# Performance work log

Measured on AMD Instinct MI355X. Metric: run time of the kernel, lower is better.

The kernel has to match this reference:

```python
import jax, jax.numpy as jnp
import numpy as np

N_NODES = 100000
N_EDGES = 800000
IN_FEATS = 128
HIDDEN = 64
SCALE = 0.5 ** 0.5  # sqrt(0.5) residual scale
BN_EPS = 1e-5


def setup_inputs() -> dict:
    key = jax.random.key(0)
    ks = jax.random.split(key, 12)
    return {
        "src": jax.random.randint(ks[0], (N_EDGES,), 0, N_NODES, dtype=jnp.int64)
        if jax.config.jax_enable_x64 else jax.random.randint(ks[0], (N_EDGES,), 0, N_NODES),
        "dst": jax.random.randint(ks[1], (N_EDGES,), 0, N_NODES),
        "x": jax.random.normal(ks[2], (N_NODES, IN_FEATS), dtype=jnp.float32),
        "fc_w": jax.random.normal(ks[3], (IN_FEATS, HIDDEN), dtype=jnp.float32) * 0.05,
        "fc_b": jax.random.normal(ks[4], (HIDDEN,), dtype=jnp.float32) * 0.05,
        "w1": jax.random.normal(ks[5], (HIDDEN, HIDDEN), dtype=jnp.float32) * 0.05,
        "b1": jax.random.normal(ks[6], (HIDDEN,), dtype=jnp.float32) * 0.05,
        "w2": jax.random.normal(ks[7], (HIDDEN, HIDDEN), dtype=jnp.float32) * 0.05,
        "b2": jax.random.normal(ks[8], (HIDDEN,), dtype=jnp.float32) * 0.05,
        "gamma": jax.random.normal(ks[9], (HIDDEN,), dtype=jnp.float32) * 0.05 + 1.0,
        "beta": jax.random.normal(ks[10], (HIDDEN,), dtype=jnp.float32) * 0.05,
    }


def _graph_conv(h, w, b, src, dst, norm_src, norm_dst, n_nodes):
    # DGL GraphConv, norm='both': y = D_in^{-1/2} A D_out^{-1/2} (h W) + b
    h = h @ w                                   # [N, H]
    m = h[src] * norm_src[:, None]              # gather + src-degree norm, [E, H]
    agg = jax.ops.segment_sum(m, dst, num_segments=n_nodes)  # scatter-add, [N, H]
    return agg * norm_dst[:, None] + b


def reference(src, dst, x, fc_w, fc_b, w1, b1, w2, b2, gamma, beta):
    n_nodes = x.shape[0]
    ones_e = jnp.ones(src.shape[0], dtype=x.dtype)
    deg_out = jnp.clip(jax.ops.segment_sum(ones_e, src, num_segments=n_nodes), 1.0)
    deg_in = jnp.clip(jax.ops.segment_sum(ones_e, dst, num_segments=n_nodes), 1.0)
    norm_src = (deg_out ** -0.5)[src]           # per-edge source normalization
    norm_dst = deg_in ** -0.5                   # per-node destination normalization

    h = x @ fc_w + fc_b                          # fc: [N, H]
    h = (h + _graph_conv(h, w1, b1, src, dst, norm_src, norm_dst, n_nodes)) * SCALE
    h = (h + _graph_conv(h, w2, b2, src, dst, norm_src, norm_dst, n_nodes)) * SCALE

    # BatchNorm1d (training-mode batch statistics over nodes, biased variance)
    mu = h.mean(axis=0)
    var = ((h - mu) ** 2).mean(axis=0)
    h = (h - mu) * jax.lax.rsqrt(var + BN_EPS) * gamma + beta
    return h
```

## Files before the change

### kernel.cpp

```cpp
#include <hip/hip_runtime.h>

#define HIDDEN 64
#define INFEAT 128
#define SCALE_C 0.70710678118654752f
#define BN_EPS 1e-5f
#define AGG_GRID 2048
#define RED_BLK 32

__device__ __forceinline__ int rli(int v, int l){ return __builtin_amdgcn_readlane(v, l); }

template<int KDIM, bool ADDB, bool FUSET>
__device__ __forceinline__ void gemm_body(int bid, const float* __restrict__ X,
    const float* __restrict__ W, const float* __restrict__ B,
    float* __restrict__ Y, const float* __restrict__ W2, float* __restrict__ T, int N)
{
  __shared__ float smem[128 * 65];
  const int tid  = threadIdx.x;
  const int lane = tid & 63;
  const int wid  = __builtin_amdgcn_readfirstlane(tid >> 6);
  const int nodehalf = wid >> 1;
  const int c0 = (wid & 1) * 32;
  const int base = bid * 128;
  const int myNode = nodehalf * 64 + lane;
  const int gnode = base + myNode;

  float acc[32];
  #pragma unroll
  for (int c = 0; c < 32; ++c) acc[c] = ADDB ? B[c0 + c] : 0.f;

  constexpr int NCHUNK = KDIM / 32;
  #pragma unroll 1
  for (int ck = 0; ck < NCHUNK; ++ck){
    __syncthreads();
    #pragma unroll
    for (int i = 0; i < 4; ++i){
      int f  = i * 256 + tid;
      int nd = f >> 3;
      int kq = f & 7;
      float4 v = make_float4(0.f, 0.f, 0.f, 0.f);
      if (base + nd < N)
        v = *(const float4*)(X + (size_t)(base + nd) * KDIM + ck * 32 + kq * 4);
      float* p = &smem[nd * 33 + kq * 4];
      p[0] = v.x; p[1] = v.y; p[2] = v.z; p[3] = v.w;
    }
    __syncthreads();
    const float* wrow = W + (size_t)ck * 32 * HIDDEN + c0;
    #pragma unroll
    for (int k = 0; k < 32; ++k){
      float xv = smem[myNode * 33 + k];
      #pragma unroll
      for (int c = 0; c < 32; ++c)
        acc[c] = fmaf(xv, wrow[k * HIDDEN + c], acc[c]);
    }
  }

  if (gnode < N){
    float4* yp = (float4*)(Y + (size_t)gnode * HIDDEN + c0);
    #pragma unroll
    for (int j = 0; j < 8; ++j)
      yp[j] = make_float4(acc[4*j], acc[4*j+1], acc[4*j+2], acc[4*j+3]);
  }

  if constexpr (FUSET){
    __syncthreads();
    #pragma unroll
    for (int c = 0; c < 32; ++c)
      smem[myNode * 65 + c0 + c] = acc[c];
    __syncthreads();
    float tacc[32];
    #pragma unroll
    for (int c = 0; c < 32; ++c) tacc[c] = 0.f;
    const float* w2r = W2 + c0;
    #pragma unroll
    for (int k = 0; k < 64; ++k){
      float hv = smem[myNode * 65 + k];
      #pragma unroll
      for (int c = 0; c < 32; ++c)
        tacc[c] = fmaf(hv, w2r[k * HIDDEN + c], tacc[c]);
    }
    if (gnode < N){
      float4* tp = (float4*)(T + (size_t)gnode * HIDDEN + c0);
      #pragma unroll
      for (int j = 0; j < 8; ++j)
        tp[j] = make_float4(tacc[4*j], tacc[4*j+1], tacc[4*j+2], tacc[4*j+3]);
    }
  }
}

__device__ __forceinline__ int role_gemm_idx(int b, int GB, int TOT, int& histIdx){
  int fb  = (int)(((long)b * GB) / TOT);
  int fb1 = (int)(((long)(b + 1) * GB) / TOT);
  histIdx = b - fb;
  return (fb1 > fb) ? fb : -1;
}

__global__ __launch_bounds__(256) void k_mega1(const int* __restrict__ dst,
    int* __restrict__ degI, int* __restrict__ rank, int E,
    const float* __restrict__ x, const float* __restrict__ fc_w,
    const float* __restrict__ fc_b, float* __restrict__ h,
    const float* __restrict__ w1, float* __restrict__ t, int N, int GB, int TOT){
  int hIdx;
  int g = role_gemm_idx(blockIdx.x, GB, TOT, hIdx);
  if (g >= 0) gemm_body<INFEAT, true, true>(g, x, fc_w, fc_b, h, w1, t, N);
  else {
    int e = hIdx * 256 + threadIdx.x;
    if (e < E) rank[e] = atomicAdd(&degI[dst[e]], 1);
  }
}

__global__ __launch_bounds__(256) void k_place2(const int* __restrict__ src,
    const int* __restrict__ dst, const int* __restrict__ rank,
    const int* __restrict__ rp, int* __restrict__ cs, int* __restrict__ degO, int E){
  int e = (blockIdx.x >> 1) * 256 + threadIdx.x;
  if (e < E){
    if (blockIdx.x & 1) atomicAdd(&degO[src[e]], 1);
    else                cs[rp[dst[e]] + rank[e]] = src[e];
  }
}

__global__ __launch_bounds__(256) void k_gemm64(const float* __restrict__ X,
    const float* __restrict__ W, float* __restrict__ Y, int N){
  gemm_body<HIDDEN, false, false>(blockIdx.x, X, W, nullptr, Y, nullptr, nullptr, N);
}

__global__ void k_scan1(const int* __restrict__ deg, int* __restrict__ bsum, int N){
  __shared__ int sh[256];
  int t = threadIdx.x;
  int i = blockIdx.x * 256 + t;
  sh[t] = (i < N) ? deg[i] : 0;
  __syncthreads();
  for (int ofs = 128; ofs > 0; ofs >>= 1){
    if (t < ofs) sh[t] += sh[t + ofs];
    __syncthreads();
  }
  if (t == 0) bsum[blockIdx.x] = sh[0];
}

__global__ void k_scan2(int* __restrict__ bsum, int NB){
  __shared__ int sh[512];
  int t = threadIdx.x;
  int v = (t < NB) ? bsum[t] : 0;
  sh[t] = v;
  __syncthreads();
  for (int ofs = 1; ofs < 512; ofs <<= 1){
    int u = (t >= ofs) ? sh[t - ofs] : 0;
    __syncthreads();
    sh[t] += u;
    __syncthreads();
  }
  if (t < NB) bsum[t] = sh[t] - v;
}

__global__ void k_scan3(const int* __restrict__ degI, const int* __restrict__ bofs,
                        int* __restrict__ rp, float* __restrict__ norm_in, int N, int E){
  __shared__ int sh[256];
  int t = threadIdx.x;
  int i = blockIdx.x * 256 + t;
  int v = (i < N) ? degI[i] : 0;
  sh[t] = v;
  __syncthreads();
  for (int ofs = 1; ofs < 256; ofs <<= 1){
    int u = (t >= ofs) ? sh[t - ofs] : 0;
    __syncthreads();
    sh[t] += u;
    __syncthreads();
  }
  if (i < N){
    int excl = sh[t] - v + bofs[blockIdx.x];
    rp[i] = excl;
    if (i == N - 1) rp[N] = E;
    norm_in[i] = rsqrtf((float)max(v, 1));
  }
}

__device__ __forceinline__ float gather_row(const int* __restrict__ rp,
    const int* __restrict__ cs, const float* __restrict__ t,
    const int* __restrict__ degO, int n, int lane){
  const int start = rp[n], end = rp[n + 1];
  float acc = 0.f;
  for (int j0 = start; j0 < end; j0 += 64){
    int cnt = end - j0; if (cnt > 64) cnt = 64;
    int sidx = (j0 + lane < end) ? cs[j0 + lane] : 0;
    int d = 0;
    for (; d + 8 <= cnt; d += 8){
      int a0 = rli(sidx, d),   a1 = rli(sidx, d+1);
      int a2 = rli(sidx, d+2), a3 = rli(sidx, d+3);
      int a4 = rli(sidx, d+4), a5 = rli(sidx, d+5);
      int a6 = rli(sidx, d+6), a7 = rli(sidx, d+7);
      float v0 = t[(size_t)a0 * HIDDEN + lane];
      float v1 = t[(size_t)a1 * HIDDEN + lane];
      float v2 = t[(size_t)a2 * HIDDEN + lane];
      float v3 = t[(size_t)a3 * HIDDEN + lane];
      float v4 = t[(size_t)a4 * HIDDEN + lane];
      float v5 = t[(size_t)a5 * HIDDEN + lane];
      float v6 = t[(size_t)a6 * HIDDEN + lane];
      float v7 = t[(size_t)a7 * HIDDEN + lane];
      float n0 = rsqrtf((float)degO[a0]);
      float n1 = rsqrtf((float)degO[a1]);
      float n2 = rsqrtf((float)degO[a2]);
      float n3 = rsqrtf((float)degO[a3]);
      float n4 = rsqrtf((float)degO[a4]);
      float n5 = rsqrtf((float)degO[a5]);
      float n6 = rsqrtf((float)degO[a6]);
      float n7 = rsqrtf((float)degO[a7]);
      acc = fmaf(v0, n0, acc); acc = fmaf(v1, n1, acc);
      acc = fmaf(v2, n2, acc); acc = fmaf(v3, n3, acc);
      acc = fmaf(v4, n4, acc); acc = fmaf(v5, n5, acc);
      acc = fmaf(v6, n6, acc); acc = fmaf(v7, n7, acc);
    }
    for (; d < cnt; ++d){
      int a = rli(sidx, d);
      acc = fmaf(t[(size_t)a * HIDDEN + lane], rsqrtf((float)degO[a]), acc);
    }
  }
  return acc;
}

template<bool BN>
__global__ __launch_bounds__(256) void k_agg(const int* __restrict__ rp, const int* __restrict__ cs,
    const float* __restrict__ t, const int* __restrict__ degO,
    const float* __restrict__ norm_in, const float* __restrict__ b,
    float* __restrict__ h, float* __restrict__ bnpart, int N)
{
  const int tid = threadIdx.x;
  const int lane = tid & 63;
  const int wv = (blockIdx.x * 256 + tid) >> 6;
  const int nw = (gridDim.x * 256) >> 6;
  const float bv = b[lane];
  float s1 = 0.f, s2 = 0.f;

  for (int n = wv; n < N; n += nw){
    float acc = gather_row(rp, cs, t, degO, n, lane);
    size_t idx = (size_t)n * HIDDEN + lane;
    float v = (h[idx] + acc * norm_in[n] + bv) * SCALE_C;
    h[idx] = v;
    if (BN){ s1 += v; s2 += v * v; }
  }

  if (BN){
    __shared__ float l1[256], l2[256];
    l1[tid] = s1; l2[tid] = s2;
    __syncthreads();
    if (tid < 64){
      float a1 = l1[tid] + l1[tid+64] + l1[tid+128] + l1[tid+192];
      float a2 = l2[tid] + l2[tid+64] + l2[tid+128] + l2[tid+192];
      bnpart[blockIdx.x * 128 + tid] = a1;
      bnpart[blockIdx.x * 128 + 64 + tid] = a2;
    }
  }
}

__global__ __launch_bounds__(256) void k_bnred(const float* __restrict__ bnpart,
    float* __restrict__ bnred, int nblk){
  int col  = threadIdx.x & 127;
  int half = threadIdx.x >> 7;
  int rows = nblk / RED_BLK;
  int r0 = blockIdx.x * rows;
  float s = 0.f;
  for (int r = half; r < rows; r += 2)
    s += bnpart[(size_t)(r0 + r) * 128 + col];
  __shared__ float sh[256];
  sh[threadIdx.x] = s;
  __syncthreads();
  if (threadIdx.x < 128)
    bnred[blockIdx.x * 128 + threadIdx.x] = sh[threadIdx.x] + sh[threadIdx.x + 128];
}

__global__ void k_bnfin(const float* __restrict__ bnred,
    const float* __restrict__ gamma, const float* __restrict__ beta,
    float* __restrict__ bnab, float invN){
  int c = threadIdx.x;
  float s1 = 0.f, s2 = 0.f;
  #pragma unroll
  for (int b = 0; b < RED_BLK; ++b){ s1 += bnred[b*128 + c]; s2 += bnred[b*128 + 64 + c]; }
  float mu  = s1 * invN;
  float var = s2 * invN - mu * mu;
  float rstd = rsqrtf(var + BN_EPS);
  float sc = gamma[c] * rstd;
  bnab[c] = sc;
  bnab[64 + c] = beta[c] - mu * sc;
}

__global__ void k_bnapply(float* __restrict__ h, const float* __restrict__ bnab, long total4){
  long i = (long)blockIdx.x * blockDim.x + threadIdx.x;
  if (i < total4){
    int c = (int)((i * 4) & 63);
    float4 v = ((float4*)h)[i];
    v.x = fmaf(v.x, bnab[c],     bnab[64 + c]);
    v.y = fmaf(v.y, bnab[c + 1], bnab[65 + c]);
    v.z = fmaf(v.z, bnab[c + 2], bnab[66 + c]);
    v.w = fmaf(v.w, bnab[c + 3], bnab[67 + c]);
    ((float4*)h)[i] = v;
  }
}

extern "C" void kernel_launch(void* const* d_in, const int* in_sizes, int n_in,
                              void* d_out, int out_size, void* d_ws, size_t ws_size,
                              hipStream_t stream){
  const int* src = (const int*)d_in[0];
  const int* dst = (const int*)d_in[1];
  const float* x     = (const float*)d_in[2];
  const float* fc_w  = (const float*)d_in[3];
  const float* fc_b  = (const float*)d_in[4];
  const float* w1    = (const float*)d_in[5];
  const float* b1    = (const float*)d_in[6];
  const float* w2    = (const float*)d_in[7];
  const float* b2    = (const float*)d_in[8];
  const float* gamma = (const float*)d_in[9];
  const float* beta  = (const float*)d_in[10];
  const int E = in_sizes[0];
  const int N = in_sizes[2] / INFEAT;
  const int NB = (N + 255) / 256;
  const int EB = (E + 255) / 256;
  const int GB = (N + 127) / 128;
  const int TOT = EB + GB;

  float* h = (float*)d_out;

  float* t        = (float*)d_ws;
  float* norm_in  = t + (size_t)N * HIDDEN;
  float* bnpart   = norm_in + N;
  float* bnred    = bnpart + AGG_GRID * 128;
  float* bnab     = bnred + RED_BLK * 128;
  int*   degO     = (int*)(bnab + 128);
  int*   degI     = degO + N;
  int*   rp       = degI + N;
  int*   bsum     = rp + N + 1;
  int*   rank     = bsum + 512;
  int*   cs       = rank + E;

  hipMemsetAsync(degO, 0, 2 * (size_t)N * sizeof(int), stream);

  k_mega1<<<TOT, 256, 0, stream>>>(dst, degI, rank, E,
                                   x, fc_w, fc_b, h, w1, t, N, GB, TOT);

  k_scan1<<<NB, 256, 0, stream>>>(degI, bsum, N);
  k_scan2<<<1, 512, 0, stream>>>(bsum, NB);
  k_scan3<<<NB, 256, 0, stream>>>(degI, bsum, rp, norm_in, N, E);

  k_place2<<<2 * EB, 256, 0, stream>>>(src, dst, rank, rp, cs, degO, E);

  k_agg<false><<<AGG_GRID, 256, 0, stream>>>(rp, cs, t, degO, norm_in, b1, h, nullptr, N);

  k_gemm64<<<GB, 256, 0, stream>>>(h, w2, t, N);
  k_agg<true><<<AGG_GRID, 256, 0, stream>>>(rp, cs, t, degO, norm_in, b2, h, bnpart, N);

  k_bnred<<<RED_BLK, 256, 0, stream>>>(bnpart, bnred, AGG_GRID);
  k_bnfin<<<1, 64, 0, stream>>>(bnred, gamma, beta, bnab, 1.0f / (float)N);
  long total4 = (long)N * HIDDEN / 4;
  k_bnapply<<<(int)((total4 + 255) / 256), 256, 0, stream>>>(h, bnab, total4);
}
```

Measured before the change: 370.4 us.

## Fuse second-layer GEMM into first aggregation and pre-scale by source norm

New measurement: 363.7 us. Within noise of the previous version (-1.8%).

```diff
diff --git a/kernel.cpp b/kernel.cpp
--- a/kernel.cpp
+++ b/kernel.cpp
@@ -8,48 +8,49 @@
 #define RED_BLK 32
 
 __device__ __forceinline__ int rli(int v, int l){ return __builtin_amdgcn_readlane(v, l); }
+__device__ __forceinline__ float rlf(float v, int l){
+  return __int_as_float(__builtin_amdgcn_readlane(__float_as_int(v), l));
+}
 
 template<int KDIM, bool ADDB, bool FUSET>
 __device__ __forceinline__ void gemm_body(int bid, const float* __restrict__ X,
     const float* __restrict__ W, const float* __restrict__ B,
     float* __restrict__ Y, const float* __restrict__ W2, float* __restrict__ T, int N)
 {
-  __shared__ float smem[128 * 65];
+  __shared__ float smem[64 * 65];
   const int tid  = threadIdx.x;
   const int lane = tid & 63;
   const int wid  = __builtin_amdgcn_readfirstlane(tid >> 6);
-  const int nodehalf = wid >> 1;
-  const int c0 = (wid & 1) * 32;
-  const int base = bid * 128;
-  const int myNode = nodehalf * 64 + lane;
-  const int gnode = base + myNode;
-
-  float acc[32];
+  const int c0 = wid * 16;
+  const int base = bid * 64;
+  const int gnode = base + lane;
+
+  float acc[16];
   #pragma unroll
-  for (int c = 0; c < 32; ++c) acc[c] = ADDB ? B[c0 + c] : 0.f;
+  for (int c = 0; c < 16; ++c) acc[c] = ADDB ? B[c0 + c] : 0.f;
 
   constexpr int NCHUNK = KDIM / 32;
   #pragma unroll 1
   for (int ck = 0; ck < NCHUNK; ++ck){
     __syncthreads();
     #pragma unroll
-    for (int i = 0; i < 4; ++i){
+    for (int i = 0; i < 2; ++i){
       int f  = i * 256 + tid;
       int nd = f >> 3;
       int kq = f & 7;
       float4 v = make_float4(0.f, 0.f, 0.f, 0.f);
       if (base + nd < N)
         v = *(const float4*)(X + (size_t)(base + nd) * KDIM + ck * 32 + kq * 4);
-      float* p = &smem[nd * 33 + kq * 4];
+      float* p = &smem[nd * 65 + kq * 4];
       p[0] = v.x; p[1] = v.y; p[2] = v.z; p[3] = v.w;
     }
     __syncthreads();
     const float* wrow = W + (size_t)ck * 32 * HIDDEN + c0;
     #pragma unroll
     for (int k = 0; k < 32; ++k){
-      float xv = smem[myNode * 33 + k];
+      float xv = smem[lane * 65 + k];
       #pragma unroll
-      for (int c = 0; c < 32; ++c)
+      for (int c = 0; c < 16; ++c)
         acc[c] = fmaf(xv, wrow[k * HIDDEN + c], acc[c]);
     }
   }
@@ -57,31 +58,30 @@
   if (gnode < N){
     float4* yp = (float4*)(Y + (size_t)gnode * HIDDEN + c0);
     #pragma unroll
-    for (int j = 0; j < 8; ++j)
+    for (int j = 0; j < 4; ++j)
       yp[j] = make_float4(acc[4*j], acc[4*j+1], acc[4*j+2], acc[4*j+3]);
   }
 
   if constexpr (FUSET){
     __syncthreads();
     #pragma unroll
-    for (int c = 0; c < 32; ++c)
-      smem[myNode * 65 + c0 + c] = acc[c];
-    __syncthreads();
-    float tacc[32];
-    #pragma unroll
-    for (int c = 0; c < 32; ++c) tacc[c] = 0.f;
+    for (int c = 0; c < 16; ++c) smem[lane * 65 + c0 + c] = acc[c];
+    __syncthreads();
+    float tacc[16];
+    #pragma unroll
+    for (int c = 0; c < 16; ++c) tacc[c] = 0.f;
     const float* w2r = W2 + c0;
     #pragma unroll
     for (int k = 0; k < 64; ++k){
-      float hv = smem[myNode * 65 + k];
+      float hv = smem[lane * 65 + k];
       #pragma unroll
-      for (int c = 0; c < 32; ++c)
+      for (int c = 0; c < 16; ++c)
         tacc[c] = fmaf(hv, w2r[k * HIDDEN + c], tacc[c]);
     }
     if (gnode < N){
       float4* tp = (float4*)(T + (size_t)gnode * HIDDEN + c0);
       #pragma unroll
-      for (int j = 0; j < 8; ++j)
+      for (int j = 0; j < 4; ++j)
         tp[j] = make_float4(tacc[4*j], tacc[4*j+1], tacc[4*j+2], tacc[4*j+3]);
     }
   }
@@ -103,18 +103,27 @@
   int g = role_gemm_idx(blockIdx.x, GB, TOT, hIdx);
   if (g >= 0) gemm_body<INFEAT, true, true>(g, x, fc_w, fc_b, h, w1, t, N);
   else {
-    int e = hIdx * 256 + threadIdx.x;
-    if (e < E) rank[e] = atomicAdd(&degI[dst[e]], 1);
-  }
-}
-
-__global__ __launch_bounds__(256) void k_place2(const int* __restrict__ src,
+    int e0 = hIdx * 1024 + threadIdx.x;
+    #pragma unroll
+    for (int i = 0; i < 4; ++i){
+      int e = e0 + i * 256;
+      if (e < E) rank[e] = atomicAdd(&degI[dst[e]], 1);
+    }
+  }
+}
+
+__global__ __launch_bounds__(256) void k_place(const int* __restrict__ src,
     const int* __restrict__ dst, const int* __restrict__ rank,
     const int* __restrict__ rp, int* __restrict__ cs, int* __restrict__ degO, int E){
-  int e = (blockIdx.x >> 1) * 256 + threadIdx.x;
-  if (e < E){
-    if (blockIdx.x & 1) atomicAdd(&degO[src[e]], 1);
-    else                cs[rp[dst[e]] + rank[e]] = src[e];
+  int e0 = blockIdx.x * 1024 + threadIdx.x;
+  #pragma unroll
+  for (int i = 0; i < 4; ++i){
+    int e = e0 + i * 256;
+    if (e < E){
+      int s = src[e];
+      cs[rp[dst[e]] + rank[e]] = s;
+      atomicAdd(&degO[s], 1);
+    }
   }
 }
 
@@ -173,6 +182,7 @@
   }
 }
 
+template<bool PRE>
 __device__ __forceinline__ float gather_row(const int* __restrict__ rp,
     const int* __restrict__ cs, const float* __restrict__ t,
     const int* __restrict__ degO, int n, int lane){
@@ -195,32 +205,40 @@
       float v5 = t[(size_t)a5 * HIDDEN + lane];
       float v6 = t[(size_t)a6 * HIDDEN + lane];
       float v7 = t[(size_t)a7 * HIDDEN + lane];
-      float n0 = rsqrtf((float)degO[a0]);
-      float n1 = rsqrtf((float)degO[a1]);
-      float n2 = rsqrtf((float)degO[a2]);
-      float n3 = rsqrtf((float)degO[a3]);
-      float n4 = rsqrtf((float)degO[a4]);
-      float n5 = rsqrtf((float)degO[a5]);
-      float n6 = rsqrtf((float)degO[a6]);
-      float n7 = rsqrtf((float)degO[a7]);
-      acc = fmaf(v0, n0, acc); acc = fmaf(v1, n1, acc);
-      acc = fmaf(v2, n2, acc); acc = fmaf(v3, n3, acc);
-      acc = fmaf(v4, n4, acc); acc = fmaf(v5, n5, acc);
-      acc = fmaf(v6, n6, acc); acc = fmaf(v7, n7, acc);
+      if (PRE){
+        acc += v0; acc += v1; acc += v2; acc += v3;
+        acc += v4; acc += v5; acc += v6; acc += v7;
+      } else {
+        float n0 = rsqrtf((float)degO[a0]);
+        float n1 = rsqrtf((float)degO[a1]);
+        float n2 = rsqrtf((float)degO[a2]);
+        float n3 = rsqrtf((float)degO[a3]);
+        float n4 = rsqrtf((float)degO[a4]);
+        float n5 = rsqrtf((float)degO[a5]);
+        float n6 = rsqrtf((float)degO[a6]);
+        float n7 = rsqrtf((float)degO[a7]);
+        acc = fmaf(v0, n0, acc); acc = fmaf(v1, n1, acc);
+        acc = fmaf(v2, n2, acc); acc = fmaf(v3, n3, acc);
+        acc = fmaf(v4, n4, acc); acc = fmaf(v5, n5, acc);
+        acc = fmaf(v6, n6, acc); acc = fmaf(v7, n7, acc);
+      }
     }
     for (; d < cnt; ++d){
       int a = rli(sidx, d);
-      acc = fmaf(t[(size_t)a * HIDDEN + lane], rsqrtf((float)degO[a]), acc);
+      float v = t[(size_t)a * HIDDEN + lane];
+      if (PRE) acc += v;
+      else     acc = fmaf(v, rsqrtf((float)degO[a]), acc);
     }
   }
   return acc;
 }
 
-template<bool BN>
-__global__ __launch_bounds__(256) void k_agg(const int* __restrict__ rp, const int* __restrict__ cs,
+template<bool BN, bool PRE, bool FUSET2>
+__global__ __launch_bounds__(256, 4) void k_agg(const int* __restrict__ rp, const int* __restrict__ cs,
     const float* __restrict__ t, const int* __restrict__ degO,
     const float* __restrict__ norm_in, const float* __restrict__ b,
-    float* __restrict__ h, float* __restrict__ bnpart, int N)
+    const float* __restrict__ w2, float* __restrict__ h,
+    float* __restrict__ t2, float* __restrict__ bnpart, int N)
 {
   const int tid = threadIdx.x;
   const int lane = tid & 63;
@@ -229,12 +247,30 @@
   const float bv = b[lane];
   float s1 = 0.f, s2 = 0.f;
 
+  float w2c[64];
+  if constexpr (FUSET2){
+    #pragma unroll
+    for (int k = 0; k < 64; ++k) w2c[k] = w2[k * HIDDEN + lane];
+  }
+
   for (int n = wv; n < N; n += nw){
-    float acc = gather_row(rp, cs, t, degO, n, lane);
+    float acc = gather_row<PRE>(rp, cs, t, degO, n, lane);
     size_t idx = (size_t)n * HIDDEN + lane;
     float v = (h[idx] + acc * norm_in[n] + bv) * SCALE_C;
     h[idx] = v;
     if (BN){ s1 += v; s2 += v * v; }
+    if constexpr (FUSET2){
+      float nout = rsqrtf((float)max(degO[n], 1));
+      float ta0 = 0.f, ta1 = 0.f, ta2 = 0.f, ta3 = 0.f;
+      #pragma unroll
+      for (int k = 0; k < 64; k += 4){
+        ta0 = fmaf(rlf(v, k),     w2c[k],     ta0);
+        ta1 = fmaf(rlf(v, k + 1), w2c[k + 1], ta1);
+        ta2 = fmaf(rlf(v, k + 2), w2c[k + 2], ta2);
+        ta3 = fmaf(rlf(v, k + 3), w2c[k + 3], ta3);
+      }
+      t2[idx] = ((ta0 + ta1) + (ta2 + ta3)) * nout;
+    }
   }
 
   if (BN){
@@ -310,15 +346,21 @@
   const float* beta  = (const float*)d_in[10];
   const int E = in_sizes[0];
   const int N = in_sizes[2] / INFEAT;
-  const int NB = (N + 255) / 256;
-  const int EB = (E + 255) / 256;
-  const int GB = (N + 127) / 128;
-  const int TOT = EB + GB;
+  const int NB  = (N + 255) / 256;
+  const int EB4 = (E + 1023) / 1024;
+  const int GB  = (N + 63) / 64;
+  const int TOT = EB4 + GB;
 
   float* h = (float*)d_out;
 
+  const size_t Nh = (size_t)N * HIDDEN;
+  size_t need = (2 * Nh + N + (size_t)AGG_GRID * 128 + RED_BLK * 128 + 128) * 4
+              + ((size_t)3 * N + 1 + 512 + 2 * (size_t)E) * 4;
+  const bool fused = ws_size >= need;
+
   float* t        = (float*)d_ws;
-  float* norm_in  = t + (size_t)N * HIDDEN;
+  float* t2       = fused ? (t + Nh) : nullptr;
+  float* norm_in  = fused ? (t2 + Nh) : (t + Nh);
   float* bnpart   = norm_in + N;
   float* bnred    = bnpart + AGG_GRID * 128;
   float* bnab     = bnred + RED_BLK * 128;
@@ -338,12 +380,20 @@
   k_scan2<<<1, 512, 0, stream>>>(bsum, NB);
   k_scan3<<<NB, 256, 0, stream>>>(degI, bsum, rp, norm_in, N, E);
 
-  k_place2<<<2 * EB, 256, 0, stream>>>(src, dst, rank, rp, cs, degO, E);
-
-  k_agg<false><<<AGG_GRID, 256, 0, stream>>>(rp, cs, t, degO, norm_in, b1, h, nullptr, N);
-
-  k_gemm64<<<GB, 256, 0, stream>>>(h, w2, t, N);
-  k_agg<true><<<AGG_GRID, 256, 0, stream>>>(rp, cs, t, degO, norm_in, b2, h, bnpart, N);
+  k_place<<<EB4, 256, 0, stream>>>(src, dst, rank, rp, cs, degO, E);
+
+  if (fused){
+    k_agg<false, false, true><<<AGG_GRID, 256, 0, stream>>>(
+        rp, cs, t, degO, norm_in, b1, w2, h, t2, nullptr, N);
+    k_agg<true, true, false><<<AGG_GRID, 256, 0, stream>>>(
+        rp, cs, t2, degO, norm_in, b2, nullptr, h, nullptr, bnpart, N);
+  } else {
+    k_agg<false, false, false><<<AGG_GRID, 256, 0, stream>>>(
+        rp, cs, t, degO, norm_in, b1, nullptr, h, nullptr, nullptr, N);
+    k_gemm64<<<GB, 256, 0, stream>>>(h, w2, t, N);
+    k_agg<true, false, false><<<AGG_GRID, 256, 0, stream>>>(
+        rp, cs, t, degO, norm_in, b2, nullptr, h, nullptr, bnpart, N);
+  }
 
   k_bnred<<<RED_BLK, 256, 0, stream>>>(bnpart, bnred, AGG_GRID);
   k_bnfin<<<1, 64, 0, stream>>>(bnred, gamma, beta, bnab, 1.0f / (float)N);
```
